# Performance work log

Measured on AMD Instinct MI355X. Metric: run time of the kernel, lower is better.

## Reference

```python
import jax, jax.numpy as jnp
import numpy as np

N = 20000   # nodes
E = 320000  # edges
C = 64      # channel multiplicity
NB = 8      # bessel basis size
NA = 4      # node attribute (species) dim
L_DIMS = (1, 3, 5)  # 2l+1 for l=0,1,2
SH = 9      # total spherical-harmonic dim
OFFS = (0, 1, 4, 9)


def setup_inputs() -> dict:
    key = jax.random.key(0)
    ks = jax.random.split(key, 11)
    s = lambda k, shape: jax.random.normal(k, shape, dtype=jnp.float32)
    return {
        "length": jax.random.uniform(ks[0], (E, NB), dtype=jnp.float32),
        "node_features": s(ks[1], (N, C)),
        "node_attributes": s(ks[2], (N, NA)),
        "edge_attributes": s(ks[3], (E, SH)),
        "W1": s(ks[4], (NB, 64)),
        "W2": s(ks[5], (64, 64)),
        "W3": s(ks[6], (64, 64)),
        "W4": s(ks[7], (64, 3 * C)),
        "Wl": s(ks[8], (3, C, C)),
        "Wsc": s(ks[9], (NA, C, C)),
        "edge_index": jax.random.randint(ks[10], (2, E), 0, N, dtype=jnp.int32),
    }


def reference(length, node_features, node_attributes, edge_attributes, W1, W2, W3, W4, Wl, Wsc, edge_index):
    sender, receiver = edge_index[0], edge_index[1]
    silu = jax.nn.silu
    # e3nn FullyConnectedNet: x @ W / sqrt(fan_in), silu between layers, no act on last
    h = silu(length @ W1 * np.float32(1.0 / np.sqrt(NB)))
    h = silu(h @ W2 * np.float32(0.125))
    h = silu(h @ W3 * np.float32(0.125))
    w = (h @ W4 * np.float32(0.125)).reshape(E, 3, C)  # per-edge TP weights [E,3,C]
    # weighted tensor product: scalar node feats x sh (0e x le -> le, uvu)
    wx = w * node_features[sender][:, None, :]          # [E,3,C]
    parts = []
    for l in range(3):
        Y = edge_attributes[:, OFFS[l]:OFFS[l + 1]]     # [E, 2l+1]
        parts.append((wx[:, l, :, None] * Y[:, None, :]).reshape(E, C * L_DIMS[l]))
    mij = jnp.concatenate(parts, axis=1)                # [E, C*9]
    # scatter_sum into receivers
    msg = jax.ops.segment_sum(mij, receiver, num_segments=N)  # [N, C*9]
    # e3nn Linear: per-l channel mix, 1/sqrt(fan_in) norm
    out_blocks = []
    o = 0
    for l in range(3):
        d = L_DIMS[l]
        blk = msg[:, o:o + C * d].reshape(N, C, d)
        out_blocks.append(jnp.einsum('num,uv->nvm', blk, Wl[l]) * np.float32(1.0 / np.sqrt(C)))
        o += C * d
    message = jnp.concatenate(out_blocks, axis=2)       # reshape_irreps -> [N, C, 9]
    # FullyConnectedTensorProduct(attr 0e, feat 0e) -> only 0e output has paths
    sc0 = jnp.einsum('na,nu,auw->nw', node_attributes, node_features, Wsc) * np.float32(1.0 / np.sqrt(NA * C))
    sc = jnp.concatenate([sc0, jnp.zeros((N, C * (SH - 1)), dtype=sc0.dtype)], axis=1)  # [N, C*9]
    return (message, sc)
```

## Files before the change

kernel.cpp:

```cpp
#include <hip/hip_runtime.h>
#include <hip/hip_fp16.h>

#define N_NODES 20000
#define N_EDGES 320000
#define MSG_ROW 576
#define MSG_OFF 11520000
#define SCAN_BS 256
#define NBLK_SCAN ((N_NODES + SCAN_BS - 1) / SCAN_BS)
#define NPAD 20032
#define MT_S (NPAD * 64)

typedef _Float16 f16;
typedef _Float16 f16x4 __attribute__((ext_vector_type(4)));
typedef _Float16 f16x8 __attribute__((ext_vector_type(8)));
typedef float f32x4 __attribute__((ext_vector_type(4)));

#define OFF_WT4 0
#define OFF_W1T 24576
#define OFF_WT2 28672
#define OFF_WT3 36864
#define OFF_H0  45056
#define OFF_HT  53248
#define LDS_TOTAL 69632
#define OFF_WXT 0

#define OFF_WLT  22528
#define OFF_WSCT 34816
#define WIMG_HALF 51200
#define WIMG_BYTES 102400
#define WIMG_BLOCKS 200

__device__ __forceinline__ float silu_f(float x) {
    return x * (1.0f / (1.0f + __expf(-x)));
}


__global__ __launch_bounds__(256)
void pre_kernel(const float* __restrict__ W1, const float* __restrict__ W2,
                const float* __restrict__ W3, const float* __restrict__ W4,
                const float* __restrict__ Wl, const float* __restrict__ Wsc,
                f16* __restrict__ img,
                const int* __restrict__ eidx, int* __restrict__ counts) {
    const int b = blockIdx.x;
    if (b >= WIMG_BLOCKS) {
        const int e = (b - WIMG_BLOCKS) * 256 + threadIdx.x;
        if (e < N_EDGES) atomicAdd(&counts[eidx[N_EDGES + e]], 1);
        return;
    }
    const int p = b * 256 + threadIdx.x;
    float v;
    if (p < 12288) {
        const int m = p >> 6, rem = p & 63, g = rem >> 3, j = rem & 7;
        const int k = ((g ^ (m & 7)) << 3) | j;
        v = W4[k * 192 + m];
    } else if (p < 14336) {
        const int q = p - 12288;
        const int m = q >> 5, rem = q & 31, g = rem >> 3, j = rem & 7;
        const int k = ((g ^ (m & 3)) << 3) | j;
        v = (k < 8) ? W1[k * 64 + m] : 0.f;
    } else if (p < 18432) {
        const int q = p - 14336;
        const int m = q >> 6, rem = q & 63, g = rem >> 3, j = rem & 7;
        const int k = ((g ^ (m & 7)) << 3) | j;
        v = W2[k * 64 + m];
    } else if (p < 22528) {
        const int q = p - 18432;
        const int m = q >> 6, rem = q & 63, g = rem >> 3, j = rem & 7;
        const int k = ((g ^ (m & 7)) << 3) | j;
        v = W3[k * 64 + m];
    } else if (p < OFF_WSCT) {
        const int q = p - OFF_WLT;
        const int l = q >> 12, r = q & 4095, vv = r >> 6, u = r & 63;
        v = Wl[(l * 64 + u) * 64 + vv];
    } else {
        const int q = p - OFF_WSCT;
        const int ww = q >> 8, kk = q & 255, a = kk >> 6, u = kk & 63;
        v = Wsc[(a * 64 + u) * 64 + ww];
    }
    img[p] = (f16)v;
}


__global__ __launch_bounds__(SCAN_BS)
void scan1_kernel(const int* __restrict__ counts, int* __restrict__ offs,
                  int* __restrict__ bsum) {
    __shared__ int sm[SCAN_BS];
    const int tid = threadIdx.x;
    const int i = blockIdx.x * SCAN_BS + tid;
    const int v = (i < N_NODES) ? counts[i] : 0;
    sm[tid] = v;
    __syncthreads();
#pragma unroll
    for (int off = 1; off < SCAN_BS; off <<= 1) {
        const int t = (tid >= off) ? sm[tid - off] : 0;
        __syncthreads();
        sm[tid] += t;
        __syncthreads();
    }
    if (i < N_NODES) offs[i] = sm[tid] - v;
    if (tid == SCAN_BS - 1) bsum[blockIdx.x] = sm[tid];
}

__global__ __launch_bounds__(SCAN_BS)
void scan3_kernel(int* __restrict__ offs, const int* __restrict__ bsum,
                  int* __restrict__ cursor) {
    __shared__ int bs[NBLK_SCAN];
    const int tid = threadIdx.x;
    if (tid < NBLK_SCAN) bs[tid] = bsum[tid];
    __syncthreads();
    int bbase = 0;
    for (int j = 0; j < blockIdx.x; ++j) bbase += bs[j];
    const int i = blockIdx.x * SCAN_BS + tid;
    if (i < N_NODES) {
        const int o = offs[i] + bbase;
        offs[i] = o;
        cursor[i] = o;
    }
    if (blockIdx.x == NBLK_SCAN - 1 && tid == SCAN_BS - 1)
        offs[N_NODES] = bbase + bs[NBLK_SCAN - 1];
}


__global__ __launch_bounds__(512, 4)
void edge_mlp_mfma(const float* __restrict__ length,
                   const float* __restrict__ nf,
                   const int*   __restrict__ eidx,
                   int* __restrict__ cursor,
                   int* __restrict__ order,
                   const f16*   __restrict__ wimg,
                   f16* __restrict__ wx)
{
    __shared__ __align__(16) char s[LDS_TOTAL];
    __shared__ int sendS[128];
    __shared__ int rankS[128];

    const int tid = threadIdx.x;
    const int ebase = blockIdx.x << 7;

    {
        const uint4* src = (const uint4*)wimg;
        uint4* dst = (uint4*)s;
#pragma unroll
        for (int i = 0; i < 6; ++i) {
            const int c = i * 512 + tid;
            if (c < 2816) dst[c] = src[c];
        }
    }
    if (tid < 128) {
        const int e = tid;
        const int eg = ebase + e;
        const float4 q0 = *(const float4*)&length[(size_t)eg * 8];
        const float4 q1 = *(const float4*)&length[(size_t)eg * 8 + 4];
        f16x8 h;
        h[0] = (f16)q0.x; h[1] = (f16)q0.y; h[2] = (f16)q0.z; h[3] = (f16)q0.w;
        h[4] = (f16)q1.x; h[5] = (f16)q1.y; h[6] = (f16)q1.z; h[7] = (f16)q1.w;
        *(f16x8*)(s + OFF_H0 + e * 64 + ((0 ^ (e & 3)) << 4)) = h;
        sendS[e] = eidx[eg];
        const int rcv = eidx[N_EDGES + eg];
        const int pos = atomicAdd(&cursor[rcv], 1);
        order[pos] = eg;
        rankS[e] = pos;
    } else {
        const int idx = tid - 128;
        const int e = idx / 3, gz = 1 + idx - (idx / 3) * 3;
        uint4 z; z.x = 0; z.y = 0; z.z = 0; z.w = 0;
        *(uint4*)(s + OFF_H0 + e * 64 + ((gz ^ (e & 3)) << 4)) = z;
    }
    __syncthreads();

    const int lane = tid & 63, w = tid >> 6;
    const int eh = w >> 2, wm = w & 3;
    const int lm = lane & 15, lg = lane >> 4;
    const int mrow = wm * 16 + lm;
    const int r0 = lg << 2;
    const int eloc0 = eh << 6;

    const f32x4 zacc = {0.f, 0.f, 0.f, 0.f};
    f32x4 acc[4];

    {
        const f16x8 a = *(const f16x8*)(s + OFF_W1T + mrow * 64 + ((lg ^ (mrow & 3)) << 4));
#pragma unroll
        for (int nt = 0; nt < 4; ++nt) {
            const int e = eloc0 + nt * 16 + lm;
            const f16x8 b = *(const f16x8*)(s + OFF_H0 + e * 64 + ((lg ^ (e & 3)) << 4));
            acc[nt] = __builtin_amdgcn_mfma_f32_16x16x32_f16(a, b, zacc, 0, 0, 0);
        }
    }
    {
        const int c = wm * 16 + r0;
#pragma unroll
        for (int nt = 0; nt < 4; ++nt) {
            const int e = eloc0 + nt * 16 + lm;
            f16x4 pk;
            pk[0] = (f16)silu_f(acc[nt][0] * 0.35355339059f);
            pk[1] = (f16)silu_f(acc[nt][1] * 0.35355339059f);
            pk[2] = (f16)silu_f(acc[nt][2] * 0.35355339059f);
            pk[3] = (f16)silu_f(acc[nt][3] * 0.35355339059f);
            *(f16x4*)(s + OFF_HT + e * 128 + (((c >> 3) ^ (e & 7)) << 4) + ((c & 7) << 1)) = pk;
        }
    }
    __syncthreads();

#pragma unroll
    for (int nt = 0; nt < 4; ++nt) acc[nt] = zacc;
#pragma unroll
    for (int kh = 0; kh < 2; ++kh) {
        const int g = (kh << 2) + lg;
        const f16x8 a = *(const f16x8*)(s + OFF_WT2 + mrow * 128 + ((g ^ (mrow & 7)) << 4));
#pragma unroll
        for (int nt = 0; nt < 4; ++nt) {
            const int e = eloc0 + nt * 16 + lm;
            const f16x8 b = *(const f16x8*)(s + OFF_HT + e * 128 + ((g ^ (e & 7)) << 4));
            acc[nt] = __builtin_amdgcn_mfma_f32_16x16x32_f16(a, b, acc[nt], 0, 0, 0);
        }
    }
    __syncthreads();
    {
        const int c = wm * 16 + r0;
#pragma unroll
        for (int nt = 0; nt < 4; ++nt) {
            const int e = eloc0 + nt * 16 + lm;
            f16x4 pk;
            pk[0] = (f16)silu_f(acc[nt][0] * 0.125f);
            pk[1] = (f16)silu_f(acc[nt][1] * 0.125f);
            pk[2] = (f16)silu_f(acc[nt][2] * 0.125f);
            pk[3] = (f16)silu_f(acc[nt][3] * 0.125f);
            *(f16x4*)(s + OFF_HT + e * 128 + (((c >> 3) ^ (e & 7)) << 4) + ((c & 7) << 1)) = pk;
        }
    }
    __syncthreads();

#pragma unroll
    for (int nt = 0; nt < 4; ++nt) acc[nt] = zacc;
#pragma unroll
    for (int kh = 0; kh < 2; ++kh) {
        const int g = (kh << 2) + lg;
        const f16x8 a = *(const f16x8*)(s + OFF_WT3 + mrow * 128 + ((g ^ (mrow & 7)) << 4));
#pragma unroll
        for (int nt = 0; nt < 4; ++nt) {
            const int e = eloc0 + nt * 16 + lm;
            const f16x8 b = *(const f16x8*)(s + OFF_HT + e * 128 + ((g ^ (e & 7)) << 4));
            acc[nt] = __builtin_amdgcn_mfma_f32_16x16x32_f16(a, b, acc[nt], 0, 0, 0);
        }
    }
    __syncthreads();
    {
        const int c = wm * 16 + r0;
#pragma unroll
        for (int nt = 0; nt < 4; ++nt) {
            const int e = eloc0 + nt * 16 + lm;
            f16x4 pk;
            pk[0] = (f16)silu_f(acc[nt][0] * 0.125f);
            pk[1] = (f16)silu_f(acc[nt][1] * 0.125f);
            pk[2] = (f16)silu_f(acc[nt][2] * 0.125f);
            pk[3] = (f16)silu_f(acc[nt][3] * 0.125f);
            *(f16x4*)(s + OFF_HT + e * 128 + (((c >> 3) ^ (e & 7)) << 4) + ((c & 7) << 1)) = pk;
        }
    }
    __syncthreads();

    f32x4 acc4[3][4];
#pragma unroll
    for (int p = 0; p < 3; ++p)
#pragma unroll
        for (int nt = 0; nt < 4; ++nt) acc4[p][nt] = zacc;
#pragma unroll
    for (int kh = 0; kh < 2; ++kh) {
        const int g = (kh << 2) + lg;
        f16x8 ap[3];
#pragma unroll
        for (int p = 0; p < 3; ++p) {
            const int m4 = p * 64 + mrow;
            ap[p] = *(const f16x8*)(s + OFF_WT4 + m4 * 128 + ((g ^ (m4 & 7)) << 4));
        }
#pragma unroll
        for (int nt = 0; nt < 4; ++nt) {
            const int e = eloc0 + nt * 16 + lm;
            const f16x8 b = *(const f16x8*)(s + OFF_HT + e * 128 + ((g ^ (e & 7)) << 4));
#pragma unroll
            for (int p = 0; p < 3; ++p)
                acc4[p][nt] = __builtin_amdgcn_mfma_f32_16x16x32_f16(ap[p], b, acc4[p][nt], 0, 0, 0);
        }
    }
    __syncthreads();

#pragma unroll
    for (int nt = 0; nt < 4; ++nt) {
        const int e = eloc0 + nt * 16 + lm;
        const int snd = sendS[e];
        const float4 nf4 = *(const float4*)&nf[(size_t)snd * 64 + wm * 16 + r0];
#pragma unroll
        for (int p = 0; p < 3; ++p) {
            const int c = p * 64 + wm * 16 + r0;
            f16x4 pk;
            pk[0] = (f16)(acc4[p][nt][0] * 0.125f * nf4.x);
            pk[1] = (f16)(acc4[p][nt][1] * 0.125f * nf4.y);
            pk[2] = (f16)(acc4[p][nt][2] * 0.125f * nf4.z);
            pk[3] = (f16)(acc4[p][nt][3] * 0.125f * nf4.w);
            *(f16x4*)(s + OFF_WXT + e * 384 + (((c >> 3) ^ (e & 7)) << 4) + ((c & 7) << 1)) = pk;
        }
    }
    __syncthreads();

#pragma unroll
    for (int it = 0; it < 6; ++it) {
        const int chunk = it * 512 + tid;
        const int e = chunk / 24, g = chunk - e * 24;
        const uint4 v = *(const uint4*)(s + OFF_WXT + e * 384 + ((g ^ (e & 7)) << 4));
        *(uint4*)((char*)wx + (size_t)rankS[e] * 384 + g * 16) = v;
    }
}


__global__ __launch_bounds__(256, 8)
void gather_kernel(const __half* __restrict__ wx,
                   const float* __restrict__ ea,
                   const int* __restrict__ offs,
                   const int* __restrict__ order,
                   f16* __restrict__ mT)
{
    const int tid = threadIdx.x;
    const int wid = tid >> 6;
    const int v   = tid & 63;
    const int n   = (blockIdx.x << 2) + wid;
    const int beg = offs[n];
    const int end = offs[n + 1];

    float a0 = 0.f, a1[3] = {0.f, 0.f, 0.f}, a2[5] = {0.f, 0.f, 0.f, 0.f, 0.f};
    int k = beg;
    for (; k + 2 <= end; k += 2) {
        const int eA = __builtin_amdgcn_readfirstlane(order[k]);
        const int eB = __builtin_amdgcn_readfirstlane(order[k + 1]);
        const __half* wrA = wx + (size_t)k * 192;
        const __half* wrB = wx + (size_t)(k + 1) * 192;
        const float xA0 = __half2float(wrA[v]);
        const float xA1 = __half2float(wrA[64 + v]);
        const float xA2 = __half2float(wrA[128 + v]);
        const float xB0 = __half2float(wrB[v]);
        const float xB1 = __half2float(wrB[64 + v]);
        const float xB2 = __half2float(wrB[128 + v]);
        const float* yA = ea + (size_t)eA * 9;
        const float* yB = ea + (size_t)eB * 9;
        a0 += xA0 * yA[0] + xB0 * yB[0];
#pragma unroll
        for (int m = 0; m < 3; ++m) a1[m] += xA1 * yA[1 + m] + xB1 * yB[1 + m];
#pragma unroll
        for (int m = 0; m < 5; ++m) a2[m] += xA2 * yA[4 + m] + xB2 * yB[4 + m];
    }
    if (k < end) {
        const int e = __builtin_amdgcn_readfirstlane(order[k]);
        const __half* wr = wx + (size_t)k * 192;
        const float x0 = __half2float(wr[v]);
        const float x1 = __half2float(wr[64 + v]);
        const float x2 = __half2float(wr[128 + v]);
        const float* y = ea + (size_t)e * 9;
        a0 += x0 * y[0];
#pragma unroll
        for (int m = 0; m < 3; ++m) a1[m] += x1 * y[1 + m];
#pragma unroll
        for (int m = 0; m < 5; ++m) a2[m] += x2 * y[4 + m];
    }

    f16* base = mT + (size_t)n * 64 + v;
    base[0] = (f16)a0;
#pragma unroll
    for (int m = 0; m < 3; ++m) base[(size_t)(1 + m) * MT_S] = (f16)a1[m];
#pragma unroll
    for (int m = 0; m < 5; ++m) base[(size_t)(4 + m) * MT_S] = (f16)a2[m];
}


__global__ __launch_bounds__(256, 2)
void node_mfma(const f16* __restrict__ wimg,
               const f16* __restrict__ mT,
               const float* __restrict__ nf,
               const float* __restrict__ na,
               float* __restrict__ out)
{
    __shared__ __align__(16) f16  mst[9 * 16 * 64];
    __shared__ __align__(16) f16  nft[16 * 64];
    __shared__ __align__(16) float nas[256];
    __shared__ __align__(16) float outb[16 * 580];

    const int tid = threadIdx.x;
    const int lane = tid & 63, w = tid >> 6;
    const int lm = lane & 15, lg = lane >> 4;
    const int r0 = lg << 2;
    const int n0 = blockIdx.x << 6;

    const f16* wlT  = wimg + OFF_WLT;
    const f16* wscT = wimg + OFF_WSCT;
    f16x8 wl[3][2];
#pragma unroll
    for (int l = 0; l < 3; ++l)
#pragma unroll
        for (int kk = 0; kk < 2; ++kk)
            wl[l][kk] = *(const f16x8*)(wlT + ((l << 6) + (w << 4) + lm) * 64 + (kk << 5) + (lg << 3));
    f16x8 wsc[8];
#pragma unroll
    for (int kg = 0; kg < 8; ++kg)
        wsc[kg] = *(const f16x8*)(wscT + ((w << 4) + lm) * 256 + (kg << 5) + (lg << 3));

    {
        const int n = n0 + (tid >> 2);
        nas[tid] = (n < N_NODES) ? na[(size_t)n * 4 + (tid & 3)] : 0.f;
    }

    const f32x4 zacc = {0.f, 0.f, 0.f, 0.f};

    for (int nt = 0; nt < 4; ++nt) {
        const int ng = n0 + (nt << 4);
        __syncthreads();

#pragma unroll
        for (int it = 0; it < 5; ++it) {
            const int c = it * 256 + tid;
            if (c < 1152) {
                const int m = c >> 7, rem = c & 127, r = rem >> 3, g = rem & 7;
                const uint4 v = *(const uint4*)(mT + (size_t)m * MT_S + (size_t)(ng + r) * 64 + (g << 3));
                *(uint4*)(&mst[m * 1024 + r * 64 + ((g ^ (r & 7)) << 3)]) = v;
            }
        }
        {
            const int r = tid >> 4, c4 = (tid & 15) << 2;
            const int n = ng + r;
            float4 v4;
            if (n < N_NODES) v4 = *(const float4*)&nf[(size_t)n * 64 + c4];
            else { v4.x = 0.f; v4.y = 0.f; v4.z = 0.f; v4.w = 0.f; }
            f16x4 h;
            h[0] = (f16)v4.x; h[1] = (f16)v4.y; h[2] = (f16)v4.z; h[3] = (f16)v4.w;
            const int g = c4 >> 3;
            *(f16x4*)&nft[r * 64 + ((g ^ (r & 7)) << 3) + (c4 & 7)] = h;
        }
        __syncthreads();

#pragma unroll
        for (int m = 0; m < 9; ++m) {
            const int l = (m == 0) ? 0 : ((m < 4) ? 1 : 2);
            f32x4 acc = zacc;
#pragma unroll
            for (int kk = 0; kk < 2; ++kk) {
                const int g = (kk << 2) + lg;
                const f16x8 b = *(const f16x8*)&mst[m * 1024 + lm * 64 + ((g ^ (lm & 7)) << 3)];
                acc = __builtin_amdgcn_mfma_f32_16x16x32_f16(wl[l][kk], b, acc, 0, 0, 0);
            }
#pragma unroll
            for (int i = 0; i < 4; ++i)
                outb[lm * 580 + ((w << 4) + r0 + i) * 9 + m] = acc[i] * 0.125f;
        }
        __syncthreads();

#pragma unroll
        for (int it = 0; it < 9; ++it) {
            const int c = it * 256 + tid;
            const int r = c / 144, q = c - r * 144;
            const int n = ng + r;
            if (n < N_NODES) {
                const float4 v = *(const float4*)&outb[r * 580 + (q << 2)];
                *(float4*)&out[(size_t)n * 576 + (q << 2)] = v;
            }
        }
        __syncthreads();

        {
            const float4 na4 = *(const float4*)&nas[((nt << 4) + lm) << 2];
            const float* nap = (const float*)&na4;
            f32x4 sacc = zacc;
#pragma unroll
            for (int kg = 0; kg < 8; ++kg) {
                const int g = ((kg & 1) << 2) + lg;
                f16x8 q = *(const f16x8*)&nft[lm * 64 + ((g ^ (lm & 7)) << 3)];
                const f16 sa = (f16)nap[kg >> 1];
                q = q * sa;
                sacc = __builtin_amdgcn_mfma_f32_16x16x32_f16(wsc[kg], q, sacc, 0, 0, 0);
            }
#pragma unroll
            for (int i = 0; i < 4; ++i)
                outb[lm * 580 + (w << 4) + r0 + i] = sacc[i] * 0.0625f;
        }
        __syncthreads();

        {
            const int r = tid >> 4, q = tid & 15;
            const int n = ng + r;
            if (n < N_NODES)
                *(float4*)&out[(size_t)MSG_OFF + (size_t)n * 576 + (q << 2)] =
                    *(const float4*)&outb[r * 580 + (q << 2)];
        }
        float4 z4; z4.x = 0.f; z4.y = 0.f; z4.z = 0.f; z4.w = 0.f;
#pragma unroll
        for (int it = 0; it < 8; ++it) {
            const int c = it * 256 + tid;
            const int r = c >> 7, q = c & 127;
            const int n = ng + r;
            if (n < N_NODES)
                *(float4*)&out[(size_t)MSG_OFF + (size_t)n * 576 + 64 + (q << 2)] = z4;
        }
    }
}


__device__ __forceinline__ void layer_accum(const float* src, const float* __restrict__ W,
                                            float a2[4][4], int c0, int e0) {
#pragma unroll
    for (int i = 0; i < 4; ++i)
#pragma unroll
        for (int j = 0; j < 4; ++j) a2[i][j] = 0.f;
#pragma unroll 8
    for (int u = 0; u < 64; ++u) {
        const float4 h4 = *(const float4*)&src[(u << 6) + e0];
        const float4 w4 = *(const float4*)&W[(u << 6) + c0];
        const float hv[4] = {h4.x, h4.y, h4.z, h4.w};
        const float wv[4] = {w4.x, w4.y, w4.z, w4.w};
#pragma unroll
        for (int i = 0; i < 4; ++i)
#pragma unroll
            for (int j = 0; j < 4; ++j) a2[i][j] += wv[i] * hv[j];
    }
}

__device__ __forceinline__ void layer_store(float* dst, const float a2[4][4],
                                            float scale, int c0, int e0) {
#pragma unroll
    for (int i = 0; i < 4; ++i) {
        float4 v;
        v.x = silu_f(a2[i][0] * scale);
        v.y = silu_f(a2[i][1] * scale);
        v.z = silu_f(a2[i][2] * scale);
        v.w = silu_f(a2[i][3] * scale);
        *(float4*)&dst[((c0 + i) << 6) + e0] = v;
    }
}

__global__ __launch_bounds__(256, 4)
void edge_kernel_atomic(const float* __restrict__ length,
                        const float* __restrict__ nf,
                        const float* __restrict__ ea,
                        const float* __restrict__ W1,
                        const float* __restrict__ W2,
                        const float* __restrict__ W3,
                        const float* __restrict__ W4,
                        const int*   __restrict__ eidx,
                        float* __restrict__ msg)
{
    __shared__ float buf[4096];
    __shared__ float lenS[512];
    __shared__ float Ys[576];
    __shared__ int   sendS[64];
    __shared__ int   recvS[64];

    const int tid = threadIdx.x;
    const int tx = tid & 15;
    const int ty = tid >> 4;
    const int c0 = tx << 2;
    const int e0 = ty << 2;
    const int ebase = blockIdx.x << 6;

    for (int i = tid; i < 512; i += 256) {
        const int e = i >> 3, k = i & 7;
        lenS[(k << 6) + e] = length[((ebase + e) << 3) + k];
    }
    for (int i = tid; i < 576; i += 256) Ys[i] = ea[ebase * 9 + i];
    if (tid < 64) {
        sendS[tid] = eidx[ebase + tid];
        recvS[tid] = eidx[N_EDGES + ebase + tid];
    }
    __syncthreads();

    {
        float a2[4][4];
#pragma unroll
        for (int i = 0; i < 4; ++i)
#pragma unroll
            for (int j = 0; j < 4; ++j) a2[i][j] = 0.f;
#pragma unroll
        for (int k = 0; k < 8; ++k) {
            const float4 h4 = *(const float4*)&lenS[(k << 6) + e0];
            const float4 w4 = *(const float4*)&W1[(k << 6) + c0];
            const float hv[4] = {h4.x, h4.y, h4.z, h4.w};
            const float wv[4] = {w4.x, w4.y, w4.z, w4.w};
#pragma unroll
            for (int i = 0; i < 4; ++i)
#pragma unroll
                for (int j = 0; j < 4; ++j) a2[i][j] += wv[i] * hv[j];
        }
        layer_store(buf, a2, 0.35355339059327373f, c0, e0);
    }
    __syncthreads();
    {
        float a2[4][4];
        layer_accum(buf, W2, a2, c0, e0);
        __syncthreads();
        layer_store(buf, a2, 0.125f, c0, e0);
    }
    __syncthreads();
    {
        float a2[4][4];
        layer_accum(buf, W3, a2, c0, e0);
        __syncthreads();
        layer_store(buf, a2, 0.125f, c0, e0);
    }
    __syncthreads();

    float wacc[3][4][4];
#pragma unroll
    for (int l = 0; l < 3; ++l)
#pragma unroll
        for (int i = 0; i < 4; ++i)
#pragma unroll
            for (int j = 0; j < 4; ++j) wacc[l][i][j] = 0.f;
#pragma unroll 4
    for (int u = 0; u < 64; ++u) {
        const float4 h4 = *(const float4*)&buf[(u << 6) + e0];
        const float hv[4] = {h4.x, h4.y, h4.z, h4.w};
#pragma unroll
        for (int l = 0; l < 3; ++l) {
            const float4 w4 = *(const float4*)&W4[u * 192 + (l << 6) + c0];
            const float wv[4] = {w4.x, w4.y, w4.z, w4.w};
#pragma unroll
            for (int i = 0; i < 4; ++i)
#pragma unroll
                for (int j = 0; j < 4; ++j) wacc[l][i][j] += wv[i] * hv[j];
        }
    }

#pragma unroll
    for (int j = 0; j < 4; ++j) {
        const int e = e0 + j;
        const int snd = sendS[e];
        const int rcv = recvS[e];
        const float4 nf4 = *(const float4*)&nf[(snd << 6) + c0];
        const float nfv[4] = {nf4.x, nf4.y, nf4.z, nf4.w};
        float* mrow = msg + rcv * MSG_ROW;
        const float y0 = Ys[e * 9 + 0];
        float y1[3], y2[5];
#pragma unroll
        for (int m = 0; m < 3; ++m) y1[m] = Ys[e * 9 + 1 + m];
#pragma unroll
        for (int m = 0; m < 5; ++m) y2[m] = Ys[e * 9 + 4 + m];
#pragma unroll
        for (int i = 0; i < 4; ++i) {
            const int c = c0 + i;
            const float wx0 = wacc[0][i][j] * 0.125f * nfv[i];
            const float wx1 = wacc[1][i][j] * 0.125f * nfv[i];
            const float wx2 = wacc[2][i][j] * 0.125f * nfv[i];
            atomicAdd(&mrow[c], wx0 * y0);
#pragma unroll
            for (int m = 0; m < 3; ++m) atomicAdd(&mrow[64 + c * 3 + m], wx1 * y1[m]);
#pragma unroll
            for (int m = 0; m < 5; ++m) atomicAdd(&mrow[256 + c * 5 + m], wx2 * y2[m]);
        }
    }
}

__global__ __launch_bounds__(256, 4)
void node_kernel(const float* __restrict__ nf,
                 const float* __restrict__ na,
                 const float* __restrict__ Wl,
                 const float* __restrict__ Wsc,
                 float* __restrict__ out)
{
    __shared__ float ms[4][576];
    __shared__ float fs[4][64];
    const int tid = threadIdx.x;
    const int wid = tid >> 6;
    const int v   = tid & 63;
    const int n   = (blockIdx.x << 2) + wid;
    const float* msg = out + MSG_OFF;

#pragma unroll
    for (int j = 0; j < 9; ++j)
        ms[wid][(j << 6) + v] = msg[n * MSG_ROW + (j << 6) + v];
    fs[wid][v] = nf[(n << 6) + v];
    __syncthreads();

    float o9[9];
#pragma unroll
    for (int j = 0; j < 9; ++j) o9[j] = 0.f;
    const float* m0 = &ms[wid][0];
    const float* m1 = &ms[wid][64];
    const float* m2 = &ms[wid][256];

#pragma unroll 8
    for (int u = 0; u < 64; ++u) {
        const float w0 = Wl[(u << 6) + v];
        const float w1 = Wl[4096 + (u << 6) + v];
        const float w2 = Wl[8192 + (u << 6) + v];
        o9[0] += m0[u] * w0;
        o9[1] += m1[u * 3 + 0] * w1;
        o9[2] += m1[u * 3 + 1] * w1;
        o9[3] += m1[u * 3 + 2] * w1;
        o9[4] += m2[u * 5 + 0] * w2;
        o9[5] += m2[u * 5 + 1] * w2;
        o9[6] += m2[u * 5 + 2] * w2;
        o9[7] += m2[u * 5 + 3] * w2;
        o9[8] += m2[u * 5 + 4] * w2;
    }
#pragma unroll
    for (int j = 0; j < 9; ++j) out[n * MSG_ROW + v * 9 + j] = o9[j] * 0.125f;

    const float b0 = na[(n << 2) + 0];
    const float b1 = na[(n << 2) + 1];
    const float b2 = na[(n << 2) + 2];
    const float b3 = na[(n << 2) + 3];
    float sacc = 0.f;
#pragma unroll 8
    for (int u = 0; u < 64; ++u) {
        const float f = fs[wid][u];
        sacc += f * (b0 * Wsc[(u << 6) + v] + b1 * Wsc[4096 + (u << 6) + v] +
                     b2 * Wsc[8192 + (u << 6) + v] + b3 * Wsc[12288 + (u << 6) + v]);
    }
    float* scrow = out + MSG_OFF + n * MSG_ROW;
    scrow[v] = sacc * 0.0625f;
#pragma unroll
    for (int j = 1; j < 9; ++j) scrow[(j << 6) + v] = 0.f;
}

extern "C" void kernel_launch(void* const* d_in, const int* in_sizes, int n_in,
                              void* d_out, int out_size, void* d_ws, size_t ws_size,
                              hipStream_t stream) {
    const float* length = (const float*)d_in[0];
    const float* nfeat  = (const float*)d_in[1];
    const float* nattr  = (const float*)d_in[2];
    const float* eattr  = (const float*)d_in[3];
    const float* W1     = (const float*)d_in[4];
    const float* W2     = (const float*)d_in[5];
    const float* W3     = (const float*)d_in[6];
    const float* W4     = (const float*)d_in[7];
    const float* Wl     = (const float*)d_in[8];
    const float* Wsc    = (const float*)d_in[9];
    const int*   eidx   = (const int*)d_in[10];
    float* out = (float*)d_out;

    f16*    wimg   = (f16*)d_ws;
    __half* wx     = (__half*)((char*)d_ws + WIMG_BYTES);
    f16*    mT     = (f16*)((char*)d_ws + WIMG_BYTES + (size_t)N_EDGES * 192 * 2);
    int*   counts  = (int*)((char*)mT + (size_t)9 * MT_S * 2);
    int*   offsets = counts + N_NODES;
    int*   cursor  = offsets + N_NODES + 1;
    int*   order   = cursor + N_NODES;
    int*   bsum    = order + N_EDGES;
    const size_t need = WIMG_BYTES + (size_t)N_EDGES * 192 * 2 + (size_t)9 * MT_S * 2 +
                        (size_t)(N_NODES * 3 + 1 + N_EDGES + 128) * 4;

    if (ws_size >= need) {
        hipMemsetAsync(counts, 0, N_NODES * sizeof(int), stream);
        pre_kernel<<<WIMG_BLOCKS + N_EDGES / 256, 256, 0, stream>>>(W1, W2, W3, W4, Wl, Wsc,
                                                                    wimg, eidx, counts);
        scan1_kernel<<<NBLK_SCAN, SCAN_BS, 0, stream>>>(counts, offsets, bsum);
        scan3_kernel<<<NBLK_SCAN, SCAN_BS, 0, stream>>>(offsets, bsum, cursor);
        edge_mlp_mfma<<<N_EDGES / 128, 512, 0, stream>>>(length, nfeat, eidx, cursor, order,
                                                         wimg, (f16*)wx);
        gather_kernel<<<N_NODES / 4, 256, 0, stream>>>(wx, eattr, offsets, order, mT);
        node_mfma<<<NPAD / 64, 256, 0, stream>>>(wimg, mT, nfeat, nattr, out);
    } else {
        hipMemsetAsync(out + MSG_OFF, 0, (size_t)N_NODES * MSG_ROW * sizeof(float), stream);
        edge_kernel_atomic<<<N_EDGES / 64, 256, 0, stream>>>(length, nfeat, eattr,
                                                             W1, W2, W3, W4, eidx,
                                                             out + MSG_OFF);
        node_kernel<<<N_NODES / 4, 256, 0, stream>>>(nfeat, nattr, Wl, Wsc, out);
    }
}
```

Baseline: 150.5 us.

## Read W4 from global memory and split the wx staging to shrink edge-kernel LDS

The edge MLP kernel no longer copies the 24 KB W4 image into LDS. Its fragments are read straight from global memory (L2/L1-cached) inside the last GEMM. The wx output staging is split into two half-block phases so the staging buffer needs only 64 edges, which cuts LDS from about 68 KB to about 44 KB per block. The aim is to allow more resident blocks per CU and to drop the W4 LDS load. The costs are global-latency loads in the W4 MFMA loop and an extra pair of barriers.

New measurement: 155.1 us. +3.0%, slower.

```diff
diff --git a/kernel.cpp b/kernel.cpp
--- a/kernel.cpp
+++ b/kernel.cpp
@@ -15,20 +15,20 @@
 typedef _Float16 f16x8 __attribute__((ext_vector_type(8)));
 typedef float f32x4 __attribute__((ext_vector_type(4)));
 
-#define OFF_WT4 0
-#define OFF_W1T 24576
-#define OFF_WT2 28672
-#define OFF_WT3 36864
-#define OFF_H0  45056
-#define OFF_HT  53248
-#define LDS_TOTAL 69632
-#define OFF_WXT 0
-
+#define IMG_WT4_B 0
 #define OFF_WLT  22528
 #define OFF_WSCT 34816
 #define WIMG_HALF 51200
 #define WIMG_BYTES 102400
 #define WIMG_BLOCKS 200
+
+#define EK_W1T 0
+#define EK_WT2 4096
+#define EK_WT3 12288
+#define EK_H0  20480
+#define EK_HT  28672
+#define EK_LDS 45056
+#define EK_WXT 0
 
 __device__ __forceinline__ float silu_f(float x) {
     return x * (1.0f / (1.0f + __expf(-x)));
@@ -130,7 +130,7 @@
                    const f16*   __restrict__ wimg,
                    f16* __restrict__ wx)
 {
-    __shared__ __align__(16) char s[LDS_TOTAL];
+    __shared__ __align__(16) char s[EK_LDS];
     __shared__ int sendS[128];
     __shared__ int rankS[128];
 
@@ -138,12 +138,12 @@
     const int ebase = blockIdx.x << 7;
 
     {
-        const uint4* src = (const uint4*)wimg;
+        const uint4* src = (const uint4*)wimg + 1536;
         uint4* dst = (uint4*)s;
 #pragma unroll
-        for (int i = 0; i < 6; ++i) {
+        for (int i = 0; i < 3; ++i) {
             const int c = i * 512 + tid;
-            if (c < 2816) dst[c] = src[c];
+            if (c < 1280) dst[c] = src[c];
         }
     }
     if (tid < 128) {
@@ -154,7 +154,7 @@
         f16x8 h;
         h[0] = (f16)q0.x; h[1] = (f16)q0.y; h[2] = (f16)q0.z; h[3] = (f16)q0.w;
         h[4] = (f16)q1.x; h[5] = (f16)q1.y; h[6] = (f16)q1.z; h[7] = (f16)q1.w;
-        *(f16x8*)(s + OFF_H0 + e * 64 + ((0 ^ (e & 3)) << 4)) = h;
+        *(f16x8*)(s + EK_H0 + e * 64 + ((0 ^ (e & 3)) << 4)) = h;
         sendS[e] = eidx[eg];
         const int rcv = eidx[N_EDGES + eg];
         const int pos = atomicAdd(&cursor[rcv], 1);
@@ -164,7 +164,7 @@
         const int idx = tid - 128;
         const int e = idx / 3, gz = 1 + idx - (idx / 3) * 3;
         uint4 z; z.x = 0; z.y = 0; z.z = 0; z.w = 0;
-        *(uint4*)(s + OFF_H0 + e * 64 + ((gz ^ (e & 3)) << 4)) = z;
+        *(uint4*)(s + EK_H0 + e * 64 + ((gz ^ (e & 3)) << 4)) = z;
     }
     __syncthreads();
 
@@ -179,11 +179,11 @@
     f32x4 acc[4];
 
     {
-        const f16x8 a = *(const f16x8*)(s + OFF_W1T + mrow * 64 + ((lg ^ (mrow & 3)) << 4));
+        const f16x8 a = *(const f16x8*)(s + EK_W1T + mrow * 64 + ((lg ^ (mrow & 3)) << 4));
 #pragma unroll
         for (int nt = 0; nt < 4; ++nt) {
             const int e = eloc0 + nt * 16 + lm;
-            const f16x8 b = *(const f16x8*)(s + OFF_H0 + e * 64 + ((lg ^ (e & 3)) << 4));
+            const f16x8 b = *(const f16x8*)(s + EK_H0 + e * 64 + ((lg ^ (e & 3)) << 4));
             acc[nt] = __builtin_amdgcn_mfma_f32_16x16x32_f16(a, b, zacc, 0, 0, 0);
         }
     }
@@ -197,7 +197,7 @@
             pk[1] = (f16)silu_f(acc[nt][1] * 0.35355339059f);
             pk[2] = (f16)silu_f(acc[nt][2] * 0.35355339059f);
             pk[3] = (f16)silu_f(acc[nt][3] * 0.35355339059f);
-            *(f16x4*)(s + OFF_HT + e * 128 + (((c >> 3) ^ (e & 7)) << 4) + ((c & 7) << 1)) = pk;
+            *(f16x4*)(s + EK_HT + e * 128 + (((c >> 3) ^ (e & 7)) << 4) + ((c & 7) << 1)) = pk;
         }
     }
     __syncthreads();
@@ -207,11 +207,11 @@
 #pragma unroll
     for (int kh = 0; kh < 2; ++kh) {
         const int g = (kh << 2) + lg;
-        const f16x8 a = *(const f16x8*)(s + OFF_WT2 + mrow * 128 + ((g ^ (mrow & 7)) << 4));
+        const f16x8 a = *(const f16x8*)(s + EK_WT2 + mrow * 128 + ((g ^ (mrow & 7)) << 4));
 #pragma unroll
         for (int nt = 0; nt < 4; ++nt) {
             const int e = eloc0 + nt * 16 + lm;
-            const f16x8 b = *(const f16x8*)(s + OFF_HT + e * 128 + ((g ^ (e & 7)) << 4));
+            const f16x8 b = *(const f16x8*)(s + EK_HT + e * 128 + ((g ^ (e & 7)) << 4));
             acc[nt] = __builtin_amdgcn_mfma_f32_16x16x32_f16(a, b, acc[nt], 0, 0, 0);
         }
     }
@@ -226,7 +226,7 @@
             pk[1] = (f16)silu_f(acc[nt][1] * 0.125f);
             pk[2] = (f16)silu_f(acc[nt][2] * 0.125f);
             pk[3] = (f16)silu_f(acc[nt][3] * 0.125f);
-            *(f16x4*)(s + OFF_HT + e * 128 + (((c >> 3) ^ (e & 7)) << 4) + ((c & 7) << 1)) = pk;
+            *(f16x4*)(s + EK_HT + e * 128 + (((c >> 3) ^ (e & 7)) << 4) + ((c & 7) << 1)) = pk;
         }
     }
     __syncthreads();
@@ -236,11 +236,11 @@
 #pragma unroll
     for (int kh = 0; kh < 2; ++kh) {
         const int g = (kh << 2) + lg;
-        const f16x8 a = *(const f16x8*)(s + OFF_WT3 + mrow * 128 + ((g ^ (mrow & 7)) << 4));
+        const f16x8 a = *(const f16x8*)(s + EK_WT3 + mrow * 128 + ((g ^ (mrow & 7)) << 4));
 #pragma unroll
         for (int nt = 0; nt < 4; ++nt) {
             const int e = eloc0 + nt * 16 + lm;
-            const f16x8 b = *(const f16x8*)(s + OFF_HT + e * 128 + ((g ^ (e & 7)) << 4));
+            const f16x8 b = *(const f16x8*)(s + EK_HT + e * 128 + ((g ^ (e & 7)) << 4));
             acc[nt] = __builtin_amdgcn_mfma_f32_16x16x32_f16(a, b, acc[nt], 0, 0, 0);
         }
     }
@@ -255,7 +255,7 @@
             pk[1] = (f16)silu_f(acc[nt][1] * 0.125f);
             pk[2] = (f16)silu_f(acc[nt][2] * 0.125f);
             pk[3] = (f16)silu_f(acc[nt][3] * 0.125f);
-            *(f16x4*)(s + OFF_HT + e * 128 + (((c >> 3) ^ (e & 7)) << 4) + ((c & 7) << 1)) = pk;
+            *(f16x4*)(s + EK_HT + e * 128 + (((c >> 3) ^ (e & 7)) << 4) + ((c & 7) << 1)) = pk;
         }
     }
     __syncthreads();
@@ -272,43 +272,48 @@
 #pragma unroll
         for (int p = 0; p < 3; ++p) {
             const int m4 = p * 64 + mrow;
-            ap[p] = *(const f16x8*)(s + OFF_WT4 + m4 * 128 + ((g ^ (m4 & 7)) << 4));
+            ap[p] = *(const f16x8*)((const char*)wimg + IMG_WT4_B + m4 * 128 + ((g ^ (m4 & 7)) << 4));
         }
 #pragma unroll
         for (int nt = 0; nt < 4; ++nt) {
             const int e = eloc0 + nt * 16 + lm;
-            const f16x8 b = *(const f16x8*)(s + OFF_HT + e * 128 + ((g ^ (e & 7)) << 4));
+            const f16x8 b = *(const f16x8*)(s + EK_HT + e * 128 + ((g ^ (e & 7)) << 4));
 #pragma unroll
             for (int p = 0; p < 3; ++p)
                 acc4[p][nt] = __builtin_amdgcn_mfma_f32_16x16x32_f16(ap[p], b, acc4[p][nt], 0, 0, 0);
         }
     }
-    __syncthreads();
-
-#pragma unroll
-    for (int nt = 0; nt < 4; ++nt) {
-        const int e = eloc0 + nt * 16 + lm;
-        const int snd = sendS[e];
-        const float4 nf4 = *(const float4*)&nf[(size_t)snd * 64 + wm * 16 + r0];
-#pragma unroll
-        for (int p = 0; p < 3; ++p) {
-            const int c = p * 64 + wm * 16 + r0;
-            f16x4 pk;
-            pk[0] = (f16)(acc4[p][nt][0] * 0.125f * nf4.x);
-            pk[1] = (f16)(acc4[p][nt][1] * 0.125f * nf4.y);
-            pk[2] = (f16)(acc4[p][nt][2] * 0.125f * nf4.z);
-            pk[3] = (f16)(acc4[p][nt][3] * 0.125f * nf4.w);
-            *(f16x4*)(s + OFF_WXT + e * 384 + (((c >> 3) ^ (e & 7)) << 4) + ((c & 7) << 1)) = pk;
-        }
-    }
-    __syncthreads();
-
-#pragma unroll
-    for (int it = 0; it < 6; ++it) {
-        const int chunk = it * 512 + tid;
-        const int e = chunk / 24, g = chunk - e * 24;
-        const uint4 v = *(const uint4*)(s + OFF_WXT + e * 384 + ((g ^ (e & 7)) << 4));
-        *(uint4*)((char*)wx + (size_t)rankS[e] * 384 + g * 16) = v;
+
+#pragma unroll
+    for (int ph = 0; ph < 2; ++ph) {
+        if (eh == ph) {
+#pragma unroll
+            for (int nt = 0; nt < 4; ++nt) {
+                const int e = eloc0 + nt * 16 + lm;
+                const int el = e - ph * 64;
+                const int snd = sendS[e];
+                const float4 nf4 = *(const float4*)&nf[(size_t)snd * 64 + wm * 16 + r0];
+#pragma unroll
+                for (int p = 0; p < 3; ++p) {
+                    const int c = p * 64 + wm * 16 + r0;
+                    f16x4 pk;
+                    pk[0] = (f16)(acc4[p][nt][0] * 0.125f * nf4.x);
+                    pk[1] = (f16)(acc4[p][nt][1] * 0.125f * nf4.y);
+                    pk[2] = (f16)(acc4[p][nt][2] * 0.125f * nf4.z);
+                    pk[3] = (f16)(acc4[p][nt][3] * 0.125f * nf4.w);
+                    *(f16x4*)(s + EK_WXT + el * 384 + (((c >> 3) ^ (el & 7)) << 4) + ((c & 7) << 1)) = pk;
+                }
+            }
+        }
+        __syncthreads();
+#pragma unroll
+        for (int it = 0; it < 3; ++it) {
+            const int chunk = it * 512 + tid;
+            const int el = chunk / 24, g = chunk - el * 24;
+            const uint4 v = *(const uint4*)(s + EK_WXT + el * 384 + ((g ^ (el & 7)) << 4));
+            *(uint4*)((char*)wx + (size_t)rankS[el + ph * 64] * 384 + g * 16) = v;
+        }
+        __syncthreads();
     }
 }
 
```
